# Kernel tuning notes

Hardware: AMD Instinct MI355X
Metric: run time of the kernel (lower is better)

The kernel has to match this reference:

```python
import jax, jax.numpy as jnp
import numpy as np

EPS = 1e-5

def _bn(x, g, b, axes):
    m = jnp.mean(x, axes, keepdims=True)
    v = jnp.var(x, axes, keepdims=True)
    return (x - m) * jax.lax.rsqrt(v + EPS) * g + b

def _fps(p, m):
    # farthest point sampling: p [B,N,3] -> int32 indices [B,m]
    B, N, _ = p.shape
    def step(carry, _):
        mind, last = carry
        lastp = jnp.take_along_axis(p, last[:, None, None], axis=1)[:, 0]  # [B,3]
        d = jnp.sum((p - lastp[:, None, :]) ** 2, axis=-1)                 # [B,N]
        mind = jnp.minimum(mind, d)
        nxt = jnp.argmax(mind, axis=1).astype(jnp.int32)
        return (mind, nxt), last
    init = (jnp.full((B, N), jnp.inf, p.dtype), jnp.zeros((B,), jnp.int32))
    _, idxs = jax.lax.scan(step, init, None, length=m)  # [m,B]
    return idxs.T

def _gather(x, idx):
    # x [B,N,C], idx [B,...] -> [B,...,C]
    B, C = x.shape[0], x.shape[-1]
    flat = idx.reshape(B, -1)
    out = jnp.take_along_axis(x, flat[:, :, None], axis=1)
    return out.reshape(idx.shape + (C,))

def _transition_down(p, h, W, g, b, stride, nsample):
    # p [B,N,3], h [B,N,C] -> new_p [B,N//stride,3], y [B,N//stride,Cout]
    B, N, _ = p.shape
    M = N // stride
    idx = _fps(p, M)
    new_p = _gather(p, idx)                                               # [B,M,3]
    d = jnp.sum((new_p[:, :, None, :] - p[:, None, :, :]) ** 2, axis=-1)  # [B,M,N]
    _, nidx = jax.lax.top_k(-d, nsample)                                  # [B,M,k]
    gp = _gather(p, nidx) - new_p[:, :, None, :]                          # rel xyz [B,M,k,3]
    gx = _gather(h, nidx)                                                 # [B,M,k,C]
    feat = jnp.concatenate([gp, gx], axis=-1)                             # with_xyz=True
    y = jnp.einsum('bmkc,cd->bmkd', feat, W)
    y = jax.nn.relu(_bn(y, g, b, (0, 1, 2)))
    return new_p, jnp.max(y, axis=2)                                      # MaxPool1d(nsample)

def _forward(x, W1, g1, b1, W2, g2, b2, W3, g3, b3, W4, g4, b4, W5, g5, b5,
             Wc1, bc1, gc1, hc1, Wc2, bc2, gc2, hc2, Wc3, bc3):
    p = x[..., :3]                                    # in_channels == 3 -> features = xyz
    h = jnp.einsum('bnc,cd->bnd', p, W1)
    h = jax.nn.relu(_bn(h, g1, b1, (0, 1)))           # enc1: stride=1
    p, h = _transition_down(p, h, W2, g2, b2, 4, 16)  # enc2
    p, h = _transition_down(p, h, W3, g3, b3, 4, 16)  # enc3
    p, h = _transition_down(p, h, W4, g4, b4, 4, 16)  # enc4
    p, h = _transition_down(p, h, W5, g5, b5, 4, 16)  # enc5
    z = jnp.mean(h, axis=1)                           # segment-mean pool -> [B,512]
    z = jax.nn.relu(_bn(z @ Wc1 + bc1, gc1, hc1, (0,)))   # Dropout = identity (eval)
    z = jax.nn.relu(_bn(z @ Wc2 + bc2, gc2, hc2, (0,)))
    return z @ Wc3 + bc3                              # [B,40]

def setup_inputs() -> dict:
    key = jax.random.key(0)
    ks = jax.random.split(key, 16)
    B, N = 16, 4096
    def lin(k, fi, fo):
        return (jax.random.normal(k, (fi, fo), jnp.float32) / np.sqrt(fi)).astype(jnp.float32)
    inp = {"x": jax.random.normal(ks[0], (B, N, 3), jnp.float32)}
    planes = [32, 64, 128, 256, 512]
    ins = [3, 3 + 32, 3 + 64, 3 + 128, 3 + 256]
    for i, (fi, fo) in enumerate(zip(ins, planes), start=1):
        inp[f"W{i}"] = lin(ks[i], fi, fo)
        inp[f"g{i}"] = jnp.ones((fo,), jnp.float32)
        inp[f"b{i}"] = jnp.zeros((fo,), jnp.float32)
    dims = [(512, 256), (256, 128), (128, 40)]
    for j, (fi, fo) in enumerate(dims, start=1):
        inp[f"Wc{j}"] = lin(ks[5 + j], fi, fo)
        inp[f"bc{j}"] = jnp.zeros((fo,), jnp.float32)
        if j < 3:
            inp[f"gc{j}"] = jnp.ones((fo,), jnp.float32)
            inp[f"hc{j}"] = jnp.zeros((fo,), jnp.float32)
    return inp

def reference(x, W1, g1, b1, W2, g2, b2, W3, g3, b3, W4, g4, b4, W5, g5, b5,
              Wc1, bc1, gc1, hc1, Wc2, bc2, gc2, hc2, Wc3, bc3):
    return _forward(x, W1, g1, b1, W2, g2, b2, W3, g3, b3, W4, g4, b4, W5, g5, b5,
                    Wc1, bc1, gc1, hc1, Wc2, bc2, gc2, hc2, Wc3, bc3)
```

## Files before the change

kernel.cpp:

```cpp
#include <hip/hip_runtime.h>
#include <math.h>
#include <float.h>

#define BN_EPS 1e-5f

__device__ __forceinline__ float sqdist_exact(float dx, float dy, float dz) {
  return __fadd_rn(__fadd_rn(__fmul_rn(dx, dx), __fmul_rn(dy, dy)), __fmul_rn(dz, dz));
}

__global__ void __launch_bounds__(256) mlp1_kernel(const float* __restrict__ x,
                                                   const float* __restrict__ W1,
                                                   float* __restrict__ h1, int rows) {
  int tid = blockIdx.x * 256 + threadIdx.x;
  int row = tid >> 5;
  int d = tid & 31;
  if (row >= rows) return;
  float x0 = x[row * 3 + 0], x1 = x[row * 3 + 1], x2 = x[row * 3 + 2];
  float acc = x0 * W1[d] + x1 * W1[32 + d] + x2 * W1[64 + d];
  h1[row * 32 + d] = acc;
}

__global__ void stats_kernel(const float* __restrict__ v, int n, int D,
                             float* __restrict__ partial) {
  int tid = blockIdx.x * blockDim.x + threadIdx.x;
  int stride = blockDim.x * gridDim.x;
  float s = 0.f, q = 0.f;
  for (int i = tid; i < n; i += stride) { float a = v[i]; s += a; q += a * a; }
  int c = tid % D;
  extern __shared__ float sm[];
  for (int i = threadIdx.x; i < 2 * D; i += blockDim.x) sm[i] = 0.f;
  __syncthreads();
  atomicAdd(&sm[c], s);
  atomicAdd(&sm[D + c], q);
  __syncthreads();
  for (int i = threadIdx.x; i < 2 * D; i += blockDim.x)
    atomicAdd(&partial[(blockIdx.x & 63) * 2 * D + i], sm[i]);
}

__global__ void finalize_kernel(const float* __restrict__ partial,
                                const float* __restrict__ g, const float* __restrict__ b,
                                float cnt, int D, float* __restrict__ ss) {
  int d = threadIdx.x;
  if (d >= D) return;
  float s = 0.f, q = 0.f;
  for (int j = 0; j < 64; j++) { s += partial[j * 2 * D + d]; q += partial[j * 2 * D + D + d]; }
  float mean = s / cnt;
  float var = q / cnt - mean * mean;
  var = fmaxf(var, 0.f);
  float sc = g[d] * rsqrtf(var + BN_EPS);
  ss[d] = sc;
  ss[D + d] = b[d] - mean * sc;
}

__global__ void bn_apply_kernel(float* __restrict__ vmax, const float* __restrict__ vmin,
                                const float* __restrict__ ss, int D, int n) {
  int tid = blockIdx.x * blockDim.x + threadIdx.x;
  int stride = blockDim.x * gridDim.x;
  for (int i = tid; i < n; i += stride) {
    int d = i % D;
    float sc = ss[d], sh = ss[D + d];
    float v = (sc >= 0.f) ? vmax[i] : vmin[i];
    vmax[i] = fmaxf(v * sc + sh, 0.f);
  }
}

#define DPP_STEP(CTRL)                                                                   \
  {                                                                                      \
    unsigned int nhi = (unsigned int)__builtin_amdgcn_update_dpp((int)khi, (int)khi,     \
                                                                 CTRL, 0xf, 0xf, false); \
    unsigned int nlo = (unsigned int)__builtin_amdgcn_update_dpp((int)klo, (int)klo,     \
                                                                 CTRL, 0xf, 0xf, false); \
    unsigned long long nk = (((unsigned long long)nhi) << 32) | nlo;                     \
    if (nk > wk) { wk = nk; khi = nhi; klo = nlo; }                                      \
  }

template <int P, int NW>
__global__ void __launch_bounds__(NW * 64) fps4_kernel(const float* __restrict__ p,
                                                       float* __restrict__ newp) {
  constexpr int BS = NW * 64;
  constexpr int N = P * BS;
  constexpr int M = N / 4;
  __shared__ float spts[N * 3];
  __shared__ float snew[NW > 1 ? M * 3 : 1];
  __shared__ unsigned long long slots[NW > 1 ? 2 * NW : 2];
  const int b = blockIdx.x;
  const int t = threadIdx.x;
  const int wv = t >> 6;
  const int lane = t & 63;
  const float* pb = p + (size_t)b * N * 3;
  float px[P], py[P], pz[P], md[P];
#pragma unroll
  for (int j = 0; j < P; j++) {
    int i = j * BS + t;
    float x = pb[3 * i], y = pb[3 * i + 1], z = pb[3 * i + 2];
    px[j] = x; py[j] = y; pz[j] = z; md[j] = INFINITY;
    spts[3 * i] = x; spts[3 * i + 1] = y; spts[3 * i + 2] = z;
  }
  float lx = pb[0], ly = pb[1], lz = pb[2];
  if (t == 0) {
    if constexpr (NW > 1) {
      snew[0] = lx; snew[1] = ly; snew[2] = lz;
    } else {
      newp[(size_t)b * M * 3 + 0] = lx;
      newp[(size_t)b * M * 3 + 1] = ly;
      newp[(size_t)b * M * 3 + 2] = lz;
    }
  }

  for (int r = 1; r < M; r++) {
    float bv; int bi;
    {
      float d0 = sqdist_exact(px[0] - lx, py[0] - ly, pz[0] - lz);
      float m0 = fminf(md[0], d0);
      md[0] = m0;
      bv = m0; bi = t;
    }
#pragma unroll
    for (int j = 1; j < P; j++) {
      float d = sqdist_exact(px[j] - lx, py[j] - ly, pz[j] - lz);
      float m = fminf(md[j], d);
      md[j] = m;
      if (m > bv) { bv = m; bi = j * BS + t; }
    }
    unsigned int khi = __float_as_uint(bv);
    unsigned int klo = ~(unsigned int)bi;
    unsigned long long wk = (((unsigned long long)khi) << 32) | klo;
    DPP_STEP(0x111);
    DPP_STEP(0x112);
    DPP_STEP(0x114);
    DPP_STEP(0x118);
    DPP_STEP(0x142);
    DPP_STEP(0x143);
    unsigned int gidx;
    if constexpr (NW == 1) {
      unsigned int wlo = (unsigned int)__builtin_amdgcn_readlane((int)wk, 63);
      gidx = ~wlo;
    } else {
      unsigned long long* base = slots + (r & 1) * NW;
      if (lane == 63) base[wv] = wk;
      __syncthreads();
      unsigned long long fk = base[0];
#pragma unroll
      for (int w = 1; w < NW; w++) {
        unsigned long long k2 = base[w];
        if (k2 > fk) fk = k2;
      }
      gidx = ~(unsigned int)fk;
    }
    lx = spts[3 * gidx];
    ly = spts[3 * gidx + 1];
    lz = spts[3 * gidx + 2];
    if (t == 0) {
      if constexpr (NW > 1) {
        snew[3 * r] = lx; snew[3 * r + 1] = ly; snew[3 * r + 2] = lz;
      } else {
        size_t o = ((size_t)b * M + r) * 3;
        newp[o] = lx; newp[o + 1] = ly; newp[o + 2] = lz;
      }
    }
  }
  if constexpr (NW > 1) {
    __syncthreads();
    for (int i = t; i < M * 3; i += BS) newp[(size_t)b * M * 3 + i] = snew[i];
  }
}

__global__ void __launch_bounds__(256) knn_kernel(const float* __restrict__ p,
                                                  const float* __restrict__ newp,
                                                  int N, int M, int BM,
                                                  int* __restrict__ nidx) {
  int gwid = (blockIdx.x * 256 + threadIdx.x) >> 6;
  int lane = threadIdx.x & 63;
  if (gwid >= BM) return;
  int b = gwid / M;
  const float* pb = p + (size_t)b * N * 3;
  float qx = newp[(size_t)gwid * 3], qy = newp[(size_t)gwid * 3 + 1], qz = newp[(size_t)gwid * 3 + 2];
  float bd[16];
  int bi[16];
#pragma unroll
  for (int s = 0; s < 16; s++) { bd[s] = INFINITY; bi[s] = 0x7FFFFFFF; }
  for (int c = lane; c < N; c += 64) {
    float d = sqdist_exact(pb[3 * c] - qx, pb[3 * c + 1] - qy, pb[3 * c + 2] - qz);
    if (d < bd[15]) {
      bd[15] = d; bi[15] = c;
#pragma unroll
      for (int s = 15; s >= 1; --s) {
        bool sw = bd[s] < bd[s - 1];
        if (sw) {
          float tf = bd[s]; bd[s] = bd[s - 1]; bd[s - 1] = tf;
          int ti = bi[s]; bi[s] = bi[s - 1]; bi[s - 1] = ti;
        }
      }
    }
  }
  int out = 0;
  for (int r = 0; r < 16; r++) {
    float v = bd[0]; int ii = bi[0];
    float mv = v; int mi = ii;
#pragma unroll
    for (int m = 1; m < 64; m <<= 1) {
      float v2 = __shfl_xor(mv, m);
      int i2 = __shfl_xor(mi, m);
      if (v2 < mv || (v2 == mv && i2 < mi)) { mv = v2; mi = i2; }
    }
    if (mi == ii) {
#pragma unroll
      for (int s = 0; s < 15; s++) { bd[s] = bd[s + 1]; bi[s] = bi[s + 1]; }
      bd[15] = INFINITY; bi[15] = 0x7FFFFFFF;
    }
    if (lane == r) out = mi;
  }
  if (lane < 16) nidx[(size_t)gwid * 16 + lane] = out;
}

__global__ void __launch_bounds__(256) gemm_kernel(
    const float* __restrict__ p, const float* __restrict__ h, const float* __restrict__ newp,
    const int* __restrict__ nidx, const float* __restrict__ W,
    float* __restrict__ ymax, float* __restrict__ ymin, float* __restrict__ partial,
    int N, int M, int BM, int Ch, int Cpad, int D, int Gseq) {
  extern __shared__ float sm[];
  int Ctot = Ch + 3;
  int TD = D < 256 ? D : 256;
  int Gpar = 256 / TD;
  float* sfeat = sm;
  float* sstat = sm + Gpar * 16 * Cpad;
  int t = threadIdx.x;
  for (int i = t; i < 2 * D; i += 256) sstat[i] = 0.f;
  int mloc = t / TD;
  int dbase = t % TD;
  int DV = D / TD;
  __syncthreads();
  for (int s = 0; s < Gseq; s++) {
    int grp0 = (blockIdx.x * Gseq + s) * Gpar;
    if (grp0 >= BM) break;
    int nf = Gpar * 16 * Cpad;
    for (int i = t; i < nf; i += 256) {
      int c = i % Cpad;
      int rk = i / Cpad;
      int k = rk & 15;
      int g = rk >> 4;
      int grp = grp0 + g;
      float val = 0.f;
      if (grp < BM && c < Ctot) {
        int b = grp / M;
        int nb = nidx[(size_t)grp * 16 + k];
        if (c < 3)
          val = p[((size_t)b * N + nb) * 3 + c] - newp[(size_t)grp * 3 + c];
        else
          val = h[((size_t)b * N + nb) * Ch + (c - 3)];
      }
      sfeat[i] = val;
    }
    __syncthreads();
    int grp = grp0 + mloc;
    bool act = grp < BM;
    const float* fr = sfeat + mloc * 16 * Cpad;
    for (int dv = 0; dv < DV; ++dv) {
      int d = dbase + (dv << 8);
      float acc[16];
#pragma unroll
      for (int k = 0; k < 16; k++) acc[k] = 0.f;
      for (int c = 0; c < Cpad; c += 4) {
        float w0 = (c < Ctot) ? W[(size_t)c * D + d] : 0.f;
        float w1 = (c + 1 < Ctot) ? W[(size_t)(c + 1) * D + d] : 0.f;
        float w2 = (c + 2 < Ctot) ? W[(size_t)(c + 2) * D + d] : 0.f;
        float w3 = (c + 3 < Ctot) ? W[(size_t)(c + 3) * D + d] : 0.f;
#pragma unroll
        for (int k = 0; k < 16; k++) {
          const float4 f = *reinterpret_cast<const float4*>(fr + k * Cpad + c);
          acc[k] += f.x * w0 + f.y * w1 + f.z * w2 + f.w * w3;
        }
      }
      if (act) {
        float ssum = 0.f, ssq = 0.f, amax = -INFINITY, amin = INFINITY;
#pragma unroll
        for (int k = 0; k < 16; k++) {
          float a = acc[k];
          ssum += a; ssq += a * a;
          amax = fmaxf(amax, a); amin = fminf(amin, a);
        }
        ymax[(size_t)grp * D + d] = amax;
        ymin[(size_t)grp * D + d] = amin;
        atomicAdd(&sstat[d], ssum);
        atomicAdd(&sstat[D + d], ssq);
      }
    }
    __syncthreads();
  }
  for (int i = t; i < 2 * D; i += 256)
    atomicAdd(&partial[(blockIdx.x & 63) * 2 * D + i], sstat[i]);
}

__global__ void __launch_bounds__(512) classifier_kernel(
    const float* __restrict__ h4,
    const float* __restrict__ Wc1, const float* __restrict__ bc1,
    const float* __restrict__ gc1, const float* __restrict__ hc1,
    const float* __restrict__ Wc2, const float* __restrict__ bc2,
    const float* __restrict__ gc2, const float* __restrict__ hc2,
    const float* __restrict__ Wc3, const float* __restrict__ bc3,
    float* __restrict__ out) {
  __shared__ float z[16 * 512];
  __shared__ float z1[16 * 256];
  __shared__ float z2[16 * 128];
  __shared__ float sc[256], sh[256];
  int t = threadIdx.x;
  for (int i = t; i < 16 * 512; i += 512) {
    int b = i >> 9, c = i & 511;
    float s = 0.f;
    for (int k = 0; k < 16; k++) s += h4[((size_t)b * 16 + k) * 512 + c];
    z[i] = s * (1.f / 16.f);
  }
  __syncthreads();
  for (int i = t; i < 16 * 256; i += 512) {
    int b = i >> 8, d = i & 255;
    float a = bc1[d];
    for (int c = 0; c < 512; c++) a += z[(b << 9) + c] * Wc1[c * 256 + d];
    z1[i] = a;
  }
  __syncthreads();
  if (t < 256) {
    float s = 0.f, q = 0.f;
    for (int b = 0; b < 16; b++) { float a = z1[(b << 8) + t]; s += a; q += a * a; }
    float mean = s * (1.f / 16.f);
    float var = fmaxf(q * (1.f / 16.f) - mean * mean, 0.f);
    float scl = gc1[t] * rsqrtf(var + BN_EPS);
    sc[t] = scl; sh[t] = hc1[t] - mean * scl;
  }
  __syncthreads();
  for (int i = t; i < 16 * 256; i += 512) {
    int d = i & 255;
    z1[i] = fmaxf(z1[i] * sc[d] + sh[d], 0.f);
  }
  __syncthreads();
  for (int i = t; i < 16 * 128; i += 512) {
    int b = i >> 7, d = i & 127;
    float a = bc2[d];
    for (int c = 0; c < 256; c++) a += z1[(b << 8) + c] * Wc2[c * 128 + d];
    z2[i] = a;
  }
  __syncthreads();
  if (t < 128) {
    float s = 0.f, q = 0.f;
    for (int b = 0; b < 16; b++) { float a = z2[(b << 7) + t]; s += a; q += a * a; }
    float mean = s * (1.f / 16.f);
    float var = fmaxf(q * (1.f / 16.f) - mean * mean, 0.f);
    float scl = gc2[t] * rsqrtf(var + BN_EPS);
    sc[t] = scl; sh[t] = hc2[t] - mean * scl;
  }
  __syncthreads();
  for (int i = t; i < 16 * 128; i += 512) {
    int d = i & 127;
    z2[i] = fmaxf(z2[i] * sc[d] + sh[d], 0.f);
  }
  __syncthreads();
  for (int i = t; i < 640; i += 512) {
    int b = i / 40, d = i % 40;
    float a = bc3[d];
    for (int c = 0; c < 128; c++) a += z2[(b << 7) + c] * Wc3[c * 40 + d];
    out[i] = a;
  }
}

extern "C" void kernel_launch(void* const* d_in, const int* in_sizes, int n_in,
                              void* d_out, int out_size, void* d_ws, size_t ws_size,
                              hipStream_t stream) {
  (void)in_sizes; (void)n_in; (void)out_size; (void)ws_size;
  const float* x   = (const float*)d_in[0];
  const float* W1  = (const float*)d_in[1];
  const float* g1  = (const float*)d_in[2];
  const float* b1  = (const float*)d_in[3];
  const float* W2  = (const float*)d_in[4];
  const float* g2  = (const float*)d_in[5];
  const float* b2  = (const float*)d_in[6];
  const float* W3  = (const float*)d_in[7];
  const float* g3  = (const float*)d_in[8];
  const float* b3  = (const float*)d_in[9];
  const float* W4  = (const float*)d_in[10];
  const float* g4  = (const float*)d_in[11];
  const float* b4  = (const float*)d_in[12];
  const float* W5  = (const float*)d_in[13];
  const float* g5  = (const float*)d_in[14];
  const float* b5  = (const float*)d_in[15];
  const float* Wc1 = (const float*)d_in[16];
  const float* bc1 = (const float*)d_in[17];
  const float* gc1 = (const float*)d_in[18];
  const float* hc1 = (const float*)d_in[19];
  const float* Wc2 = (const float*)d_in[20];
  const float* bc2 = (const float*)d_in[21];
  const float* gc2 = (const float*)d_in[22];
  const float* hc2 = (const float*)d_in[23];
  const float* Wc3 = (const float*)d_in[24];
  const float* bc3 = (const float*)d_in[25];
  float* out = (float*)d_out;

  float* ws = (float*)d_ws;
  float* HA   = ws;
  float* HB   = HA + 2097152;
  float* YMIN = HB + 1048576;
  float* NP1  = YMIN + 1048576;
  float* NP2  = NP1 + 49152;
  float* NP3  = NP2 + 12288;
  float* NP4  = NP3 + 3072;
  int*   NIDX = (int*)(NP4 + 768);
  float* PART = (float*)(NIDX + 262144);
  float* SS   = PART + 5 * 65536;

  hipMemsetAsync(PART, 0, 5 * 65536 * sizeof(float), stream);

  mlp1_kernel<<<(65536 * 32) / 256, 256, 0, stream>>>(x, W1, HA, 65536);
  stats_kernel<<<256, 256, 2 * 32 * sizeof(float), stream>>>(HA, 65536 * 32, 32, PART);
  finalize_kernel<<<1, 32, 0, stream>>>(PART, g1, b1, 65536.f, 32, SS);
  bn_apply_kernel<<<512, 256, 0, stream>>>(HA, HA, SS, 32, 65536 * 32);

  fps4_kernel<8, 8><<<16, 512, 0, stream>>>(x, NP1);
  knn_kernel<<<(16384 + 3) / 4, 256, 0, stream>>>(x, NP1, 4096, 1024, 16384, NIDX);
  gemm_kernel<<<512, 256, (4 * 16 * 36 + 2 * 64) * sizeof(float), stream>>>(
      x, HA, NP1, NIDX, W2, HB, YMIN, PART + 65536, 4096, 1024, 16384, 32, 36, 64, 8);
  finalize_kernel<<<1, 64, 0, stream>>>(PART + 65536, g2, b2, (float)(16384 * 16), 64, SS + 1024);
  bn_apply_kernel<<<512, 256, 0, stream>>>(HB, YMIN, SS + 1024, 64, 16384 * 64);

  fps4_kernel<16, 1><<<16, 64, 0, stream>>>(NP1, NP2);
  knn_kernel<<<(4096 + 3) / 4, 256, 0, stream>>>(NP1, NP2, 1024, 256, 4096, NIDX);
  gemm_kernel<<<512, 256, (2 * 16 * 68 + 2 * 128) * sizeof(float), stream>>>(
      NP1, HB, NP2, NIDX, W3, HA, YMIN, PART + 2 * 65536, 1024, 256, 4096, 64, 68, 128, 4);
  finalize_kernel<<<1, 128, 0, stream>>>(PART + 2 * 65536, g3, b3, (float)(4096 * 16), 128, SS + 2048);
  bn_apply_kernel<<<512, 256, 0, stream>>>(HA, YMIN, SS + 2048, 128, 4096 * 128);

  fps4_kernel<4, 1><<<16, 64, 0, stream>>>(NP2, NP3);
  knn_kernel<<<(1024 + 3) / 4, 256, 0, stream>>>(NP2, NP3, 256, 64, 1024, NIDX);
  gemm_kernel<<<512, 256, (16 * 132 + 2 * 256) * sizeof(float), stream>>>(
      NP2, HA, NP3, NIDX, W4, HB, YMIN, PART + 3 * 65536, 256, 64, 1024, 128, 132, 256, 2);
  finalize_kernel<<<1, 256, 0, stream>>>(PART + 3 * 65536, g4, b4, (float)(1024 * 16), 256, SS + 3072);
  bn_apply_kernel<<<512, 256, 0, stream>>>(HB, YMIN, SS + 3072, 256, 1024 * 256);

  fps4_kernel<1, 1><<<16, 64, 0, stream>>>(NP3, NP4);
  knn_kernel<<<(256 + 3) / 4, 256, 0, stream>>>(NP3, NP4, 64, 16, 256, NIDX);
  gemm_kernel<<<256, 256, (16 * 260 + 2 * 512) * sizeof(float), stream>>>(
      NP3, HB, NP4, NIDX, W5, HA, YMIN, PART + 4 * 65536, 64, 16, 256, 256, 260, 512, 1);
  finalize_kernel<<<1, 512, 0, stream>>>(PART + 4 * 65536, g5, b5, (float)(256 * 16), 512, SS + 4096);
  bn_apply_kernel<<<512, 256, 0, stream>>>(HA, YMIN, SS + 4096, 512, 256 * 512);

  classifier_kernel<<<1, 512, 0, stream>>>(HA, Wc1, bc1, gc1, hc1, Wc2, bc2, gc2, hc2, Wc3, bc3, out);
}
```

Before: 1.614 ms.

## Carry winner coordinates through FPS argmax reduction instead of shared-memory lookup

The farthest-point-sampling kernel now tracks the coordinates of each thread's best candidate and forwards them with the argmax key. Single-wave blocks read the winner's coordinates with readlane, and multi-wave blocks merge per-wave winners with DPP instead of a serial shared-memory scan. This removes the shared point copy and a dependent LDS load from every iteration. The first-level FPS also moves from 8 waves with 8 points per thread to 4 waves with 16 points per thread, adding register pressure and per-thread serial work in exchange for cheaper cross-wave reduction.

```diff
diff --git a/kernel.cpp b/kernel.cpp
--- a/kernel.cpp
+++ b/kernel.cpp
@@ -74,15 +74,34 @@
     if (nk > wk) { wk = nk; khi = nhi; klo = nlo; }                                      \
   }
 
+#define QP_MERGE(CTRL)                                                                    \
+  {                                                                                       \
+    unsigned int nhi = (unsigned int)__builtin_amdgcn_update_dpp((int)mhi, (int)mhi,      \
+                                                                 CTRL, 0xf, 0xf, false);  \
+    unsigned int nlo = (unsigned int)__builtin_amdgcn_update_dpp((int)mlo, (int)mlo,      \
+                                                                 CTRL, 0xf, 0xf, false);  \
+    int nxi = __builtin_amdgcn_update_dpp(__float_as_int(mx), __float_as_int(mx),         \
+                                          CTRL, 0xf, 0xf, false);                         \
+    int nyi = __builtin_amdgcn_update_dpp(__float_as_int(my2), __float_as_int(my2),       \
+                                          CTRL, 0xf, 0xf, false);                         \
+    int nzi = __builtin_amdgcn_update_dpp(__float_as_int(mz), __float_as_int(mz),         \
+                                          CTRL, 0xf, 0xf, false);                         \
+    unsigned long long ck = (((unsigned long long)mhi) << 32) | mlo;                      \
+    unsigned long long nk = (((unsigned long long)nhi) << 32) | nlo;                      \
+    if (nk > ck) {                                                                        \
+      mhi = nhi; mlo = nlo;                                                               \
+      mx = __int_as_float(nxi); my2 = __int_as_float(nyi); mz = __int_as_float(nzi);      \
+    }                                                                                     \
+  }
+
 template <int P, int NW>
-__global__ void __launch_bounds__(NW * 64) fps4_kernel(const float* __restrict__ p,
+__global__ void __launch_bounds__(NW * 64) fps5_kernel(const float* __restrict__ p,
                                                        float* __restrict__ newp) {
   constexpr int BS = NW * 64;
   constexpr int N = P * BS;
   constexpr int M = N / 4;
-  __shared__ float spts[N * 3];
-  __shared__ float snew[NW > 1 ? M * 3 : 1];
-  __shared__ unsigned long long slots[NW > 1 ? 2 * NW : 2];
+  __shared__ __align__(32) float slots[NW > 1 ? 2 * NW * 8 : 8];
+  __shared__ float snew[NW > 1 ? M * 3 : 3];
   const int b = blockIdx.x;
   const int t = threadIdx.x;
   const int wv = t >> 6;
@@ -92,9 +111,8 @@
 #pragma unroll
   for (int j = 0; j < P; j++) {
     int i = j * BS + t;
-    float x = pb[3 * i], y = pb[3 * i + 1], z = pb[3 * i + 2];
-    px[j] = x; py[j] = y; pz[j] = z; md[j] = INFINITY;
-    spts[3 * i] = x; spts[3 * i + 1] = y; spts[3 * i + 2] = z;
+    px[j] = pb[3 * i]; py[j] = pb[3 * i + 1]; pz[j] = pb[3 * i + 2];
+    md[j] = INFINITY;
   }
   float lx = pb[0], ly = pb[1], lz = pb[2];
   if (t == 0) {
@@ -108,22 +126,25 @@
   }
 
   for (int r = 1; r < M; r++) {
-    float bv; int bi;
+    float bv, bx, by, bz; int bi;
     {
       float d0 = sqdist_exact(px[0] - lx, py[0] - ly, pz[0] - lz);
       float m0 = fminf(md[0], d0);
       md[0] = m0;
-      bv = m0; bi = t;
+      bv = m0; bi = t; bx = px[0]; by = py[0]; bz = pz[0];
     }
 #pragma unroll
     for (int j = 1; j < P; j++) {
       float d = sqdist_exact(px[j] - lx, py[j] - ly, pz[j] - lz);
       float m = fminf(md[j], d);
       md[j] = m;
-      if (m > bv) { bv = m; bi = j * BS + t; }
+      if (m > bv) {
+        bv = m; bi = j * BS + t; bx = px[j]; by = py[j]; bz = pz[j];
+      }
     }
     unsigned int khi = __float_as_uint(bv);
     unsigned int klo = ~(unsigned int)bi;
+    const unsigned int myhi = khi, mylo = klo;
     unsigned long long wk = (((unsigned long long)khi) << 32) | klo;
     DPP_STEP(0x111);
     DPP_STEP(0x112);
@@ -131,31 +152,36 @@
     DPP_STEP(0x118);
     DPP_STEP(0x142);
     DPP_STEP(0x143);
-    unsigned int gidx;
+    unsigned int whi = (unsigned int)__builtin_amdgcn_readlane((int)(wk >> 32), 63);
+    unsigned int wlo = (unsigned int)__builtin_amdgcn_readlane((int)wk, 63);
+
     if constexpr (NW == 1) {
-      unsigned int wlo = (unsigned int)__builtin_amdgcn_readlane((int)wk, 63);
-      gidx = ~wlo;
-    } else {
-      unsigned long long* base = slots + (r & 1) * NW;
-      if (lane == 63) base[wv] = wk;
-      __syncthreads();
-      unsigned long long fk = base[0];
-#pragma unroll
-      for (int w = 1; w < NW; w++) {
-        unsigned long long k2 = base[w];
-        if (k2 > fk) fk = k2;
-      }
-      gidx = ~(unsigned int)fk;
-    }
-    lx = spts[3 * gidx];
-    ly = spts[3 * gidx + 1];
-    lz = spts[3 * gidx + 2];
-    if (t == 0) {
-      if constexpr (NW > 1) {
-        snew[3 * r] = lx; snew[3 * r + 1] = ly; snew[3 * r + 2] = lz;
-      } else {
+      int owner = (int)((~wlo) & 63u);
+      lx = __int_as_float(__builtin_amdgcn_readlane(__float_as_int(bx), owner));
+      ly = __int_as_float(__builtin_amdgcn_readlane(__float_as_int(by), owner));
+      lz = __int_as_float(__builtin_amdgcn_readlane(__float_as_int(bz), owner));
+      if (t == 0) {
         size_t o = ((size_t)b * M + r) * 3;
         newp[o] = lx; newp[o + 1] = ly; newp[o + 2] = lz;
+      }
+    } else {
+      float* base = slots + (r & 1) * NW * 8;
+      if (myhi == whi && mylo == wlo) {
+        float4 v = make_float4(__uint_as_float(whi), __uint_as_float(wlo), bx, by);
+        *reinterpret_cast<float4*>(base + wv * 8) = v;
+        base[wv * 8 + 4] = bz;
+      }
+      __syncthreads();
+      const float* sl = base + (lane & (NW - 1)) * 8;
+      const float4 s4 = *reinterpret_cast<const float4*>(sl);
+      float mz = sl[4];
+      unsigned int mhi = __float_as_uint(s4.x), mlo = __float_as_uint(s4.y);
+      float mx = s4.z, my2 = s4.w;
+      if constexpr (NW >= 2) QP_MERGE(0xB1);
+      if constexpr (NW >= 4) QP_MERGE(0x4E);
+      lx = mx; ly = my2; lz = mz;
+      if (t == 0) {
+        snew[3 * r] = lx; snew[3 * r + 1] = ly; snew[3 * r + 2] = lz;
       }
     }
   }
@@ -412,28 +438,28 @@
   finalize_kernel<<<1, 32, 0, stream>>>(PART, g1, b1, 65536.f, 32, SS);
   bn_apply_kernel<<<512, 256, 0, stream>>>(HA, HA, SS, 32, 65536 * 32);
 
-  fps4_kernel<8, 8><<<16, 512, 0, stream>>>(x, NP1);
+  fps5_kernel<16, 4><<<16, 256, 0, stream>>>(x, NP1);
   knn_kernel<<<(16384 + 3) / 4, 256, 0, stream>>>(x, NP1, 4096, 1024, 16384, NIDX);
   gemm_kernel<<<512, 256, (4 * 16 * 36 + 2 * 64) * sizeof(float), stream>>>(
       x, HA, NP1, NIDX, W2, HB, YMIN, PART + 65536, 4096, 1024, 16384, 32, 36, 64, 8);
   finalize_kernel<<<1, 64, 0, stream>>>(PART + 65536, g2, b2, (float)(16384 * 16), 64, SS + 1024);
   bn_apply_kernel<<<512, 256, 0, stream>>>(HB, YMIN, SS + 1024, 64, 16384 * 64);
 
-  fps4_kernel<16, 1><<<16, 64, 0, stream>>>(NP1, NP2);
+  fps5_kernel<16, 1><<<16, 64, 0, stream>>>(NP1, NP2);
   knn_kernel<<<(4096 + 3) / 4, 256, 0, stream>>>(NP1, NP2, 1024, 256, 4096, NIDX);
   gemm_kernel<<<512, 256, (2 * 16 * 68 + 2 * 128) * sizeof(float), stream>>>(
       NP1, HB, NP2, NIDX, W3, HA, YMIN, PART + 2 * 65536, 1024, 256, 4096, 64, 68, 128, 4);
   finalize_kernel<<<1, 128, 0, stream>>>(PART + 2 * 65536, g3, b3, (float)(4096 * 16), 128, SS + 2048);
   bn_apply_kernel<<<512, 256, 0, stream>>>(HA, YMIN, SS + 2048, 128, 4096 * 128);
 
-  fps4_kernel<4, 1><<<16, 64, 0, stream>>>(NP2, NP3);
+  fps5_kernel<4, 1><<<16, 64, 0, stream>>>(NP2, NP3);
   knn_kernel<<<(1024 + 3) / 4, 256, 0, stream>>>(NP2, NP3, 256, 64, 1024, NIDX);
   gemm_kernel<<<512, 256, (16 * 132 + 2 * 256) * sizeof(float), stream>>>(
       NP2, HA, NP3, NIDX, W4, HB, YMIN, PART + 3 * 65536, 256, 64, 1024, 128, 132, 256, 2);
   finalize_kernel<<<1, 256, 0, stream>>>(PART + 3 * 65536, g4, b4, (float)(1024 * 16), 256, SS + 3072);
   bn_apply_kernel<<<512, 256, 0, stream>>>(HB, YMIN, SS + 3072, 256, 1024 * 256);
 
-  fps4_kernel<1, 1><<<16, 64, 0, stream>>>(NP3, NP4);
+  fps5_kernel<1, 1><<<16, 64, 0, stream>>>(NP3, NP4);
   knn_kernel<<<(256 + 3) / 4, 256, 0, stream>>>(NP3, NP4, 64, 16, 256, NIDX);
   gemm_kernel<<<256, 256, (16 * 260 + 2 * 512) * sizeof(float), stream>>>(
       NP3, HB, NP4, NIDX, W5, HA, YMIN, PART + 4 * 65536, 64, 16, 256, 256, 260, 512, 1);
```

Result: slower. 1.904 ms (+18.0%).

## Fuse whole encoder into persistent megakernel overlapping FPS with worker stages

Applied to the files above, without the earlier changes.

Replaces the roughly twenty separate launches with one persistent kernel. Sixteen blocks run all four farthest-point-sampling levels back to back, chaining levels 2-4 in a single wavefront via readlane. The remaining 240 worker blocks run the MLP, kNN, gather-GEMM and batch-norm stages, separated by device-wide atomic barriers and per-level FPS ready flags. This lets the serial FPS chain overlap the MLP/BN and kNN/GEMM work and removes launch gaps. The cost is a deadlock risk if all 256 blocks are not co-resident, spin-wait overhead, and a fixed worker count for every stage.

```diff
diff --git a/kernel.cpp b/kernel.cpp
--- a/kernel.cpp
+++ b/kernel.cpp
@@ -3,65 +3,12 @@
 #include <float.h>
 
 #define BN_EPS 1e-5f
+#define WB 240
+#define FB 16
+#define TPB 512
 
 __device__ __forceinline__ float sqdist_exact(float dx, float dy, float dz) {
   return __fadd_rn(__fadd_rn(__fmul_rn(dx, dx), __fmul_rn(dy, dy)), __fmul_rn(dz, dz));
-}
-
-__global__ void __launch_bounds__(256) mlp1_kernel(const float* __restrict__ x,
-                                                   const float* __restrict__ W1,
-                                                   float* __restrict__ h1, int rows) {
-  int tid = blockIdx.x * 256 + threadIdx.x;
-  int row = tid >> 5;
-  int d = tid & 31;
-  if (row >= rows) return;
-  float x0 = x[row * 3 + 0], x1 = x[row * 3 + 1], x2 = x[row * 3 + 2];
-  float acc = x0 * W1[d] + x1 * W1[32 + d] + x2 * W1[64 + d];
-  h1[row * 32 + d] = acc;
-}
-
-__global__ void stats_kernel(const float* __restrict__ v, int n, int D,
-                             float* __restrict__ partial) {
-  int tid = blockIdx.x * blockDim.x + threadIdx.x;
-  int stride = blockDim.x * gridDim.x;
-  float s = 0.f, q = 0.f;
-  for (int i = tid; i < n; i += stride) { float a = v[i]; s += a; q += a * a; }
-  int c = tid % D;
-  extern __shared__ float sm[];
-  for (int i = threadIdx.x; i < 2 * D; i += blockDim.x) sm[i] = 0.f;
-  __syncthreads();
-  atomicAdd(&sm[c], s);
-  atomicAdd(&sm[D + c], q);
-  __syncthreads();
-  for (int i = threadIdx.x; i < 2 * D; i += blockDim.x)
-    atomicAdd(&partial[(blockIdx.x & 63) * 2 * D + i], sm[i]);
-}
-
-__global__ void finalize_kernel(const float* __restrict__ partial,
-                                const float* __restrict__ g, const float* __restrict__ b,
-                                float cnt, int D, float* __restrict__ ss) {
-  int d = threadIdx.x;
-  if (d >= D) return;
-  float s = 0.f, q = 0.f;
-  for (int j = 0; j < 64; j++) { s += partial[j * 2 * D + d]; q += partial[j * 2 * D + D + d]; }
-  float mean = s / cnt;
-  float var = q / cnt - mean * mean;
-  var = fmaxf(var, 0.f);
-  float sc = g[d] * rsqrtf(var + BN_EPS);
-  ss[d] = sc;
-  ss[D + d] = b[d] - mean * sc;
-}
-
-__global__ void bn_apply_kernel(float* __restrict__ vmax, const float* __restrict__ vmin,
-                                const float* __restrict__ ss, int D, int n) {
-  int tid = blockIdx.x * blockDim.x + threadIdx.x;
-  int stride = blockDim.x * gridDim.x;
-  for (int i = tid; i < n; i += stride) {
-    int d = i % D;
-    float sc = ss[d], sh = ss[D + d];
-    float v = (sc >= 0.f) ? vmax[i] : vmin[i];
-    vmax[i] = fmaxf(v * sc + sh, 0.f);
-  }
 }
 
 #define DPP_STEP(CTRL)                                                                   \
@@ -74,40 +21,108 @@
     if (nk > wk) { wk = nk; khi = nhi; klo = nlo; }                                      \
   }
 
-template <int P, int NW>
-__global__ void __launch_bounds__(NW * 64) fps4_kernel(const float* __restrict__ p,
-                                                       float* __restrict__ newp) {
-  constexpr int BS = NW * 64;
-  constexpr int N = P * BS;
-  constexpr int M = N / 4;
-  __shared__ float spts[N * 3];
-  __shared__ float snew[NW > 1 ? M * 3 : 1];
-  __shared__ unsigned long long slots[NW > 1 ? 2 * NW : 2];
-  const int b = blockIdx.x;
-  const int t = threadIdx.x;
-  const int wv = t >> 6;
-  const int lane = t & 63;
-  const float* pb = p + (size_t)b * N * 3;
-  float px[P], py[P], pz[P], md[P];
-#pragma unroll
-  for (int j = 0; j < P; j++) {
+struct MegaParams {
+  const float* x;
+  const float *W1, *g1, *b1;
+  const float *W2, *g2, *b2;
+  const float *W3, *g3, *b3;
+  const float *W4, *g4, *b4;
+  const float *W5, *g5, *b5;
+  float *HA, *HB, *YMIN;
+  float *NP1, *NP2, *NP3, *NP4;
+  int *NIDX1, *NIDX2, *NIDX3, *NIDX4;
+  float* PART;
+  int* SYNC;
+};
+
+__device__ __forceinline__ void worker_bar(int* cnt, int phase, int t) {
+  __syncthreads();
+  if (t == 0) {
+    __threadfence();
+    __hip_atomic_fetch_add(&cnt[phase], 1, __ATOMIC_RELEASE, __HIP_MEMORY_SCOPE_AGENT);
+    while (__hip_atomic_load(&cnt[phase], __ATOMIC_ACQUIRE, __HIP_MEMORY_SCOPE_AGENT) < WB)
+      __builtin_amdgcn_s_sleep(16);
+  }
+  __syncthreads();
+}
+
+__device__ __forceinline__ void wait_np(int* np, int k, int t) {
+  if (t == 0)
+    while (__hip_atomic_load(&np[k], __ATOMIC_ACQUIRE, __HIP_MEMORY_SCOPE_AGENT) < FB)
+      __builtin_amdgcn_s_sleep(16);
+  __syncthreads();
+}
+
+template <int PP>
+__device__ void fps_w0(const float* src, float* dstG, float* dstL, int lane, int* flag) {
+  constexpr int N = PP * 64, M = N / 4;
+  float px[PP], py[PP], pz[PP], md[PP];
+#pragma unroll
+  for (int j = 0; j < PP; j++) {
+    int i = j * 64 + lane;
+    px[j] = src[3 * i]; py[j] = src[3 * i + 1]; pz[j] = src[3 * i + 2];
+    md[j] = INFINITY;
+  }
+  float lx = src[0], ly = src[1], lz = src[2];
+  if (lane == 0) {
+    dstG[0] = lx; dstG[1] = ly; dstG[2] = lz;
+    if (dstL) { dstL[0] = lx; dstL[1] = ly; dstL[2] = lz; }
+  }
+  for (int r = 1; r < M; r++) {
+    float bv, bx, by, bz; int bi;
+    {
+      float d0 = sqdist_exact(px[0] - lx, py[0] - ly, pz[0] - lz);
+      float m0 = fminf(md[0], d0);
+      md[0] = m0;
+      bv = m0; bi = lane; bx = px[0]; by = py[0]; bz = pz[0];
+    }
+#pragma unroll
+    for (int j = 1; j < PP; j++) {
+      float d = sqdist_exact(px[j] - lx, py[j] - ly, pz[j] - lz);
+      float m = fminf(md[j], d);
+      md[j] = m;
+      if (m > bv) { bv = m; bi = j * 64 + lane; bx = px[j]; by = py[j]; bz = pz[j]; }
+    }
+    unsigned int khi = __float_as_uint(bv);
+    unsigned int klo = ~(unsigned int)bi;
+    unsigned long long wk = (((unsigned long long)khi) << 32) | klo;
+    DPP_STEP(0x111); DPP_STEP(0x112); DPP_STEP(0x114);
+    DPP_STEP(0x118); DPP_STEP(0x142); DPP_STEP(0x143);
+    unsigned int wlo = (unsigned int)__builtin_amdgcn_readlane((int)wk, 63);
+    int owner = (int)((~wlo) & 63u);
+    lx = __int_as_float(__builtin_amdgcn_readlane(__float_as_int(bx), owner));
+    ly = __int_as_float(__builtin_amdgcn_readlane(__float_as_int(by), owner));
+    lz = __int_as_float(__builtin_amdgcn_readlane(__float_as_int(bz), owner));
+    if (lane == 0) {
+      dstG[3 * r] = lx; dstG[3 * r + 1] = ly; dstG[3 * r + 2] = lz;
+      if (dstL) { dstL[3 * r] = lx; dstL[3 * r + 1] = ly; dstL[3 * r + 2] = lz; }
+    }
+  }
+  if (lane == 0) {
+    __threadfence();
+    __hip_atomic_fetch_add(flag, 1, __ATOMIC_RELEASE, __HIP_MEMORY_SCOPE_AGENT);
+  }
+}
+
+__device__ void fps_role(const MegaParams& P, float* smem, int b, int t) {
+  constexpr int P1 = 8, BS = 512, N1 = 4096, M1 = 1024;
+  float* spts = smem;
+  float* snew = smem + 12288;
+  unsigned long long* slots = (unsigned long long*)(smem + 15360);
+  const int wv = t >> 6, lane = t & 63;
+  const float* pb = P.x + (size_t)b * N1 * 3;
+  float px[P1], py[P1], pz[P1], md[P1];
+#pragma unroll
+  for (int j = 0; j < P1; j++) {
     int i = j * BS + t;
-    float x = pb[3 * i], y = pb[3 * i + 1], z = pb[3 * i + 2];
-    px[j] = x; py[j] = y; pz[j] = z; md[j] = INFINITY;
-    spts[3 * i] = x; spts[3 * i + 1] = y; spts[3 * i + 2] = z;
+    float xx = pb[3 * i], yy = pb[3 * i + 1], zz = pb[3 * i + 2];
+    px[j] = xx; py[j] = yy; pz[j] = zz; md[j] = INFINITY;
+    spts[3 * i] = xx; spts[3 * i + 1] = yy; spts[3 * i + 2] = zz;
   }
   float lx = pb[0], ly = pb[1], lz = pb[2];
-  if (t == 0) {
-    if constexpr (NW > 1) {
-      snew[0] = lx; snew[1] = ly; snew[2] = lz;
-    } else {
-      newp[(size_t)b * M * 3 + 0] = lx;
-      newp[(size_t)b * M * 3 + 1] = ly;
-      newp[(size_t)b * M * 3 + 2] = lz;
-    }
-  }
-
-  for (int r = 1; r < M; r++) {
+  if (t == 0) { snew[0] = lx; snew[1] = ly; snew[2] = lz; }
+
+  for (int r = 1; r < M1; r++) {
     float bv; int bi;
     {
       float d0 = sqdist_exact(px[0] - lx, py[0] - ly, pz[0] - lz);
@@ -116,7 +131,7 @@
       bv = m0; bi = t;
     }
 #pragma unroll
-    for (int j = 1; j < P; j++) {
+    for (int j = 1; j < P1; j++) {
       float d = sqdist_exact(px[j] - lx, py[j] - ly, pz[j] - lz);
       float m = fminf(md[j], d);
       md[j] = m;
@@ -125,116 +140,140 @@
     unsigned int khi = __float_as_uint(bv);
     unsigned int klo = ~(unsigned int)bi;
     unsigned long long wk = (((unsigned long long)khi) << 32) | klo;
-    DPP_STEP(0x111);
-    DPP_STEP(0x112);
-    DPP_STEP(0x114);
-    DPP_STEP(0x118);
-    DPP_STEP(0x142);
-    DPP_STEP(0x143);
-    unsigned int gidx;
-    if constexpr (NW == 1) {
-      unsigned int wlo = (unsigned int)__builtin_amdgcn_readlane((int)wk, 63);
-      gidx = ~wlo;
-    } else {
-      unsigned long long* base = slots + (r & 1) * NW;
-      if (lane == 63) base[wv] = wk;
-      __syncthreads();
-      unsigned long long fk = base[0];
-#pragma unroll
-      for (int w = 1; w < NW; w++) {
-        unsigned long long k2 = base[w];
-        if (k2 > fk) fk = k2;
-      }
-      gidx = ~(unsigned int)fk;
-    }
-    lx = spts[3 * gidx];
-    ly = spts[3 * gidx + 1];
-    lz = spts[3 * gidx + 2];
-    if (t == 0) {
-      if constexpr (NW > 1) {
-        snew[3 * r] = lx; snew[3 * r + 1] = ly; snew[3 * r + 2] = lz;
-      } else {
-        size_t o = ((size_t)b * M + r) * 3;
-        newp[o] = lx; newp[o + 1] = ly; newp[o + 2] = lz;
-      }
-    }
-  }
-  if constexpr (NW > 1) {
+    DPP_STEP(0x111); DPP_STEP(0x112); DPP_STEP(0x114);
+    DPP_STEP(0x118); DPP_STEP(0x142); DPP_STEP(0x143);
+    unsigned long long* base = slots + (r & 1) * 8;
+    if (lane == 63) base[wv] = wk;
     __syncthreads();
-    for (int i = t; i < M * 3; i += BS) newp[(size_t)b * M * 3 + i] = snew[i];
-  }
-}
-
-__global__ void __launch_bounds__(256) knn_kernel(const float* __restrict__ p,
-                                                  const float* __restrict__ newp,
-                                                  int N, int M, int BM,
-                                                  int* __restrict__ nidx) {
-  int gwid = (blockIdx.x * 256 + threadIdx.x) >> 6;
-  int lane = threadIdx.x & 63;
-  if (gwid >= BM) return;
-  int b = gwid / M;
-  const float* pb = p + (size_t)b * N * 3;
-  float qx = newp[(size_t)gwid * 3], qy = newp[(size_t)gwid * 3 + 1], qz = newp[(size_t)gwid * 3 + 2];
-  float bd[16];
-  int bi[16];
-#pragma unroll
-  for (int s = 0; s < 16; s++) { bd[s] = INFINITY; bi[s] = 0x7FFFFFFF; }
-  for (int c = lane; c < N; c += 64) {
-    float d = sqdist_exact(pb[3 * c] - qx, pb[3 * c + 1] - qy, pb[3 * c + 2] - qz);
-    if (d < bd[15]) {
-      bd[15] = d; bi[15] = c;
-#pragma unroll
-      for (int s = 15; s >= 1; --s) {
-        bool sw = bd[s] < bd[s - 1];
-        if (sw) {
-          float tf = bd[s]; bd[s] = bd[s - 1]; bd[s - 1] = tf;
-          int ti = bi[s]; bi[s] = bi[s - 1]; bi[s - 1] = ti;
+    unsigned long long fk = base[0];
+#pragma unroll
+    for (int w = 1; w < 8; w++) {
+      unsigned long long k2 = base[w];
+      if (k2 > fk) fk = k2;
+    }
+    unsigned int gidx = ~(unsigned int)fk;
+    lx = spts[3 * gidx]; ly = spts[3 * gidx + 1]; lz = spts[3 * gidx + 2];
+    if (t == 0) { snew[3 * r] = lx; snew[3 * r + 1] = ly; snew[3 * r + 2] = lz; }
+  }
+  __syncthreads();
+  for (int i = t; i < M1 * 3; i += BS) P.NP1[(size_t)b * M1 * 3 + i] = snew[i];
+  __syncthreads();
+  if (t == 0) {
+    __threadfence();
+    __hip_atomic_fetch_add(&P.SYNC[0], 1, __ATOMIC_RELEASE, __HIP_MEMORY_SCOPE_AGENT);
+  }
+  if (t < 64) {
+    float* snewB = smem;
+    float* snewC = smem + 1024;
+    fps_w0<16>(snew, P.NP2 + (size_t)b * 256 * 3, snewB, lane, &P.SYNC[1]);
+    fps_w0<4>(snewB, P.NP3 + (size_t)b * 64 * 3, snewC, lane, &P.SYNC[2]);
+    fps_w0<1>(snewC, P.NP4 + (size_t)b * 16 * 3, (float*)0, lane, &P.SYNC[3]);
+  }
+}
+
+__device__ void mlp_w(const MegaParams& P, float* smem, int wid, int t, int bslot) {
+  float s = 0.f, q = 0.f;
+  int tid0 = wid * TPB + t;
+  int d0 = tid0 & 31;
+  for (int i = tid0; i < 65536 * 32; i += WB * TPB) {
+    int row = i >> 5, d = i & 31;
+    float x0 = P.x[row * 3], x1 = P.x[row * 3 + 1], x2 = P.x[row * 3 + 2];
+    float a = x0 * P.W1[d] + x1 * P.W1[32 + d] + x2 * P.W1[64 + d];
+    P.HA[i] = a; s += a; q += a * a;
+  }
+  float* sm2 = smem;
+  for (int i = t; i < 64; i += TPB) sm2[i] = 0.f;
+  __syncthreads();
+  atomicAdd(&sm2[d0], s);
+  atomicAdd(&sm2[32 + d0], q);
+  __syncthreads();
+  for (int i = t; i < 64; i += TPB) atomicAdd(&P.PART[bslot * 64 + i], sm2[i]);
+}
+
+__device__ void ss_compute(const float* partial, const float* g, const float* bb,
+                           float cnt, int D, float* ssl, int t) {
+  for (int d = t; d < D; d += TPB) {
+    float s = 0.f, q = 0.f;
+    for (int j = 0; j < 64; j++) { s += partial[j * 2 * D + d]; q += partial[j * 2 * D + D + d]; }
+    float mean = s / cnt;
+    float var = fmaxf(q / cnt - mean * mean, 0.f);
+    float sc = g[d] * rsqrtf(var + BN_EPS);
+    ssl[d] = sc; ssl[D + d] = bb[d] - mean * sc;
+  }
+  __syncthreads();
+}
+
+__device__ void bn_w(float* vmax, const float* vmin, const float* ssl, int D, int n,
+                     int wid, int t) {
+  for (int i = wid * TPB + t; i < n; i += WB * TPB) {
+    int d = i & (D - 1);
+    float sc = ssl[d], sh = ssl[D + d];
+    float v = (sc >= 0.f) ? vmax[i] : vmin[i];
+    vmax[i] = fmaxf(v * sc + sh, 0.f);
+  }
+}
+
+__device__ void knn_w(const float* p, const float* newp, int N, int M, int BM,
+                      int* nidx, int wid, int t) {
+  int gw = wid * 8 + (t >> 6);
+  int lane = t & 63;
+  for (int q = gw; q < BM; q += WB * 8) {
+    int b = q / M;
+    const float* pb = p + (size_t)b * N * 3;
+    float qx = newp[(size_t)q * 3], qy = newp[(size_t)q * 3 + 1], qz = newp[(size_t)q * 3 + 2];
+    float bd[16]; int bi[16];
+#pragma unroll
+    for (int s = 0; s < 16; s++) { bd[s] = INFINITY; bi[s] = 0x7FFFFFFF; }
+    for (int c = lane; c < N; c += 64) {
+      float d = sqdist_exact(pb[3 * c] - qx, pb[3 * c + 1] - qy, pb[3 * c + 2] - qz);
+      if (d < bd[15]) {
+        bd[15] = d; bi[15] = c;
+#pragma unroll
+        for (int s = 15; s >= 1; --s) {
+          if (bd[s] < bd[s - 1]) {
+            float tf = bd[s]; bd[s] = bd[s - 1]; bd[s - 1] = tf;
+            int ti = bi[s]; bi[s] = bi[s - 1]; bi[s - 1] = ti;
+          }
         }
       }
     }
-  }
-  int out = 0;
-  for (int r = 0; r < 16; r++) {
-    float v = bd[0]; int ii = bi[0];
-    float mv = v; int mi = ii;
-#pragma unroll
-    for (int m = 1; m < 64; m <<= 1) {
-      float v2 = __shfl_xor(mv, m);
-      int i2 = __shfl_xor(mi, m);
-      if (v2 < mv || (v2 == mv && i2 < mi)) { mv = v2; mi = i2; }
-    }
-    if (mi == ii) {
-#pragma unroll
-      for (int s = 0; s < 15; s++) { bd[s] = bd[s + 1]; bi[s] = bi[s + 1]; }
-      bd[15] = INFINITY; bi[15] = 0x7FFFFFFF;
-    }
-    if (lane == r) out = mi;
-  }
-  if (lane < 16) nidx[(size_t)gwid * 16 + lane] = out;
-}
-
-__global__ void __launch_bounds__(256) gemm_kernel(
-    const float* __restrict__ p, const float* __restrict__ h, const float* __restrict__ newp,
-    const int* __restrict__ nidx, const float* __restrict__ W,
-    float* __restrict__ ymax, float* __restrict__ ymin, float* __restrict__ partial,
-    int N, int M, int BM, int Ch, int Cpad, int D, int Gseq) {
-  extern __shared__ float sm[];
+    int out = 0;
+    for (int r = 0; r < 16; r++) {
+      float v = bd[0]; int ii = bi[0];
+      float mv = v; int mi = ii;
+#pragma unroll
+      for (int m = 1; m < 64; m <<= 1) {
+        float v2 = __shfl_xor(mv, m);
+        int i2 = __shfl_xor(mi, m);
+        if (v2 < mv || (v2 == mv && i2 < mi)) { mv = v2; mi = i2; }
+      }
+      if (mi == ii) {
+#pragma unroll
+        for (int s = 0; s < 15; s++) { bd[s] = bd[s + 1]; bi[s] = bi[s + 1]; }
+        bd[15] = INFINITY; bi[15] = 0x7FFFFFFF;
+      }
+      if (lane == r) out = mi;
+    }
+    if (lane < 16) nidx[(size_t)q * 16 + lane] = out;
+  }
+}
+
+__device__ void gemm_w(const float* p, const float* h, const float* newp,
+                       const int* nidx, const float* W,
+                       float* ymax, float* ymin, float* partial,
+                       int N, int M, int BM, int Ch, int Cpad, int D,
+                       int wid, int t, float* smem, int bslot) {
   int Ctot = Ch + 3;
-  int TD = D < 256 ? D : 256;
-  int Gpar = 256 / TD;
-  float* sfeat = sm;
-  float* sstat = sm + Gpar * 16 * Cpad;
-  int t = threadIdx.x;
-  for (int i = t; i < 2 * D; i += 256) sstat[i] = 0.f;
-  int mloc = t / TD;
-  int dbase = t % TD;
-  int DV = D / TD;
-  __syncthreads();
-  for (int s = 0; s < Gseq; s++) {
-    int grp0 = (blockIdx.x * Gseq + s) * Gpar;
-    if (grp0 >= BM) break;
+  int Gpar = TPB / D;
+  float* sfeat = smem;
+  float* sstat = smem + 8192;
+  for (int i = t; i < 2 * D; i += TPB) sstat[i] = 0.f;
+  int mloc = t / D;
+  int d = t % D;
+  __syncthreads();
+  for (int grp0 = wid * Gpar; grp0 < BM; grp0 += WB * Gpar) {
     int nf = Gpar * 16 * Cpad;
-    for (int i = t; i < nf; i += 256) {
+    for (int i = t; i < nf; i += TPB) {
       int c = i % Cpad;
       int rk = i / Cpad;
       int k = rk & 15;
@@ -255,40 +294,96 @@
     int grp = grp0 + mloc;
     bool act = grp < BM;
     const float* fr = sfeat + mloc * 16 * Cpad;
-    for (int dv = 0; dv < DV; ++dv) {
-      int d = dbase + (dv << 8);
-      float acc[16];
-#pragma unroll
-      for (int k = 0; k < 16; k++) acc[k] = 0.f;
-      for (int c = 0; c < Cpad; c += 4) {
-        float w0 = (c < Ctot) ? W[(size_t)c * D + d] : 0.f;
-        float w1 = (c + 1 < Ctot) ? W[(size_t)(c + 1) * D + d] : 0.f;
-        float w2 = (c + 2 < Ctot) ? W[(size_t)(c + 2) * D + d] : 0.f;
-        float w3 = (c + 3 < Ctot) ? W[(size_t)(c + 3) * D + d] : 0.f;
-#pragma unroll
-        for (int k = 0; k < 16; k++) {
-          const float4 f = *reinterpret_cast<const float4*>(fr + k * Cpad + c);
-          acc[k] += f.x * w0 + f.y * w1 + f.z * w2 + f.w * w3;
-        }
+    float acc[16];
+#pragma unroll
+    for (int k = 0; k < 16; k++) acc[k] = 0.f;
+    for (int c = 0; c < Cpad; c += 4) {
+      float w0 = (c < Ctot) ? W[(size_t)c * D + d] : 0.f;
+      float w1 = (c + 1 < Ctot) ? W[(size_t)(c + 1) * D + d] : 0.f;
+      float w2 = (c + 2 < Ctot) ? W[(size_t)(c + 2) * D + d] : 0.f;
+      float w3 = (c + 3 < Ctot) ? W[(size_t)(c + 3) * D + d] : 0.f;
+#pragma unroll
+      for (int k = 0; k < 16; k++) {
+        const float4 f = *reinterpret_cast<const float4*>(fr + k * Cpad + c);
+        acc[k] += f.x * w0 + f.y * w1 + f.z * w2 + f.w * w3;
       }
-      if (act) {
-        float ssum = 0.f, ssq = 0.f, amax = -INFINITY, amin = INFINITY;
-#pragma unroll
-        for (int k = 0; k < 16; k++) {
-          float a = acc[k];
-          ssum += a; ssq += a * a;
-          amax = fmaxf(amax, a); amin = fminf(amin, a);
-        }
-        ymax[(size_t)grp * D + d] = amax;
-        ymin[(size_t)grp * D + d] = amin;
-        atomicAdd(&sstat[d], ssum);
-        atomicAdd(&sstat[D + d], ssq);
+    }
+    if (act) {
+      float ssum = 0.f, ssq = 0.f, amax = -INFINITY, amin = INFINITY;
+#pragma unroll
+      for (int k = 0; k < 16; k++) {
+        float a = acc[k];
+        ssum += a; ssq += a * a;
+        amax = fmaxf(amax, a); amin = fminf(amin, a);
       }
+      ymax[(size_t)grp * D + d] = amax;
+      ymin[(size_t)grp * D + d] = amin;
+      atomicAdd(&sstat[d], ssum);
+      atomicAdd(&sstat[D + d], ssq);
     }
     __syncthreads();
   }
-  for (int i = t; i < 2 * D; i += 256)
-    atomicAdd(&partial[(blockIdx.x & 63) * 2 * D + i], sstat[i]);
+  for (int i = t; i < 2 * D; i += TPB)
+    atomicAdd(&partial[bslot * 2 * D + i], sstat[i]);
+}
+
+__device__ void worker_role(const MegaParams& P, float* smem, int wid, int t, int bslot) {
+  int* np = P.SYNC;
+  int* cnt = P.SYNC + 4;
+  float* ssl = smem;
+
+  mlp_w(P, smem, wid, t, bslot);
+  worker_bar(cnt, 0, t);
+  ss_compute(P.PART, P.g1, P.b1, 65536.f, 32, ssl, t);
+  bn_w(P.HA, P.HA, ssl, 32, 65536 * 32, wid, t);
+  worker_bar(cnt, 1, t);
+
+  wait_np(np, 0, t);
+  knn_w(P.x, P.NP1, 4096, 1024, 16384, P.NIDX1, wid, t);
+  worker_bar(cnt, 2, t);
+  gemm_w(P.x, P.HA, P.NP1, P.NIDX1, P.W2, P.HB, P.YMIN, P.PART + 65536,
+         4096, 1024, 16384, 32, 36, 64, wid, t, smem, bslot);
+  worker_bar(cnt, 3, t);
+
+  ss_compute(P.PART + 65536, P.g2, P.b2, (float)(16384 * 16), 64, ssl, t);
+  bn_w(P.HB, P.YMIN, ssl, 64, 16384 * 64, wid, t);
+  wait_np(np, 1, t);
+  knn_w(P.NP1, P.NP2, 1024, 256, 4096, P.NIDX2, wid, t);
+  worker_bar(cnt, 4, t);
+  gemm_w(P.NP1, P.HB, P.NP2, P.NIDX2, P.W3, P.HA, P.YMIN, P.PART + 2 * 65536,
+         1024, 256, 4096, 64, 68, 128, wid, t, smem, bslot);
+  worker_bar(cnt, 5, t);
+
+  ss_compute(P.PART + 2 * 65536, P.g3, P.b3, (float)(4096 * 16), 128, ssl, t);
+  bn_w(P.HA, P.YMIN, ssl, 128, 4096 * 128, wid, t);
+  wait_np(np, 2, t);
+  knn_w(P.NP2, P.NP3, 256, 64, 1024, P.NIDX3, wid, t);
+  worker_bar(cnt, 6, t);
+  gemm_w(P.NP2, P.HA, P.NP3, P.NIDX3, P.W4, P.HB, P.YMIN, P.PART + 3 * 65536,
+         256, 64, 1024, 128, 132, 256, wid, t, smem, bslot);
+  worker_bar(cnt, 7, t);
+
+  ss_compute(P.PART + 3 * 65536, P.g4, P.b4, (float)(1024 * 16), 256, ssl, t);
+  bn_w(P.HB, P.YMIN, ssl, 256, 1024 * 256, wid, t);
+  wait_np(np, 3, t);
+  knn_w(P.NP3, P.NP4, 64, 16, 256, P.NIDX4, wid, t);
+  worker_bar(cnt, 8, t);
+  gemm_w(P.NP3, P.HB, P.NP4, P.NIDX4, P.W5, P.HA, P.YMIN, P.PART + 4 * 65536,
+         64, 16, 256, 256, 260, 512, wid, t, smem, bslot);
+  worker_bar(cnt, 9, t);
+
+  ss_compute(P.PART + 4 * 65536, P.g5, P.b5, (float)(256 * 16), 512, ssl, t);
+  bn_w(P.HA, P.YMIN, ssl, 512, 256 * 512, wid, t);
+}
+
+__global__ void __launch_bounds__(TPB, 4) mega_kernel(MegaParams P) {
+  __shared__ __align__(16) float smem[15872];
+  int t = threadIdx.x;
+  if (blockIdx.x < FB) {
+    fps_role(P, smem, blockIdx.x, t);
+  } else {
+    worker_role(P, smem, blockIdx.x - FB, t, blockIdx.x & 63);
+  }
 }
 
 __global__ void __launch_bounds__(512) classifier_kernel(
@@ -365,22 +460,13 @@
                               void* d_out, int out_size, void* d_ws, size_t ws_size,
                               hipStream_t stream) {
   (void)in_sizes; (void)n_in; (void)out_size; (void)ws_size;
-  const float* x   = (const float*)d_in[0];
-  const float* W1  = (const float*)d_in[1];
-  const float* g1  = (const float*)d_in[2];
-  const float* b1  = (const float*)d_in[3];
-  const float* W2  = (const float*)d_in[4];
-  const float* g2  = (const float*)d_in[5];
-  const float* b2  = (const float*)d_in[6];
-  const float* W3  = (const float*)d_in[7];
-  const float* g3  = (const float*)d_in[8];
-  const float* b3  = (const float*)d_in[9];
-  const float* W4  = (const float*)d_in[10];
-  const float* g4  = (const float*)d_in[11];
-  const float* b4  = (const float*)d_in[12];
-  const float* W5  = (const float*)d_in[13];
-  const float* g5  = (const float*)d_in[14];
-  const float* b5  = (const float*)d_in[15];
+  MegaParams P;
+  P.x  = (const float*)d_in[0];
+  P.W1 = (const float*)d_in[1];  P.g1 = (const float*)d_in[2];  P.b1 = (const float*)d_in[3];
+  P.W2 = (const float*)d_in[4];  P.g2 = (const float*)d_in[5];  P.b2 = (const float*)d_in[6];
+  P.W3 = (const float*)d_in[7];  P.g3 = (const float*)d_in[8];  P.b3 = (const float*)d_in[9];
+  P.W4 = (const float*)d_in[10]; P.g4 = (const float*)d_in[11]; P.b4 = (const float*)d_in[12];
+  P.W5 = (const float*)d_in[13]; P.g5 = (const float*)d_in[14]; P.b5 = (const float*)d_in[15];
   const float* Wc1 = (const float*)d_in[16];
   const float* bc1 = (const float*)d_in[17];
   const float* gc1 = (const float*)d_in[18];
@@ -394,51 +480,24 @@
   float* out = (float*)d_out;
 
   float* ws = (float*)d_ws;
-  float* HA   = ws;
-  float* HB   = HA + 2097152;
-  float* YMIN = HB + 1048576;
-  float* NP1  = YMIN + 1048576;
-  float* NP2  = NP1 + 49152;
-  float* NP3  = NP2 + 12288;
-  float* NP4  = NP3 + 3072;
-  int*   NIDX = (int*)(NP4 + 768);
-  float* PART = (float*)(NIDX + 262144);
-  float* SS   = PART + 5 * 65536;
-
-  hipMemsetAsync(PART, 0, 5 * 65536 * sizeof(float), stream);
-
-  mlp1_kernel<<<(65536 * 32) / 256, 256, 0, stream>>>(x, W1, HA, 65536);
-  stats_kernel<<<256, 256, 2 * 32 * sizeof(float), stream>>>(HA, 65536 * 32, 32, PART);
-  finalize_kernel<<<1, 32, 0, stream>>>(PART, g1, b1, 65536.f, 32, SS);
-  bn_apply_kernel<<<512, 256, 0, stream>>>(HA, HA, SS, 32, 65536 * 32);
-
-  fps4_kernel<8, 8><<<16, 512, 0, stream>>>(x, NP1);
-  knn_kernel<<<(16384 + 3) / 4, 256, 0, stream>>>(x, NP1, 4096, 1024, 16384, NIDX);
-  gemm_kernel<<<512, 256, (4 * 16 * 36 + 2 * 64) * sizeof(float), stream>>>(
-      x, HA, NP1, NIDX, W2, HB, YMIN, PART + 65536, 4096, 1024, 16384, 32, 36, 64, 8);
-  finalize_kernel<<<1, 64, 0, stream>>>(PART + 65536, g2, b2, (float)(16384 * 16), 64, SS + 1024);
-  bn_apply_kernel<<<512, 256, 0, stream>>>(HB, YMIN, SS + 1024, 64, 16384 * 64);
-
-  fps4_kernel<16, 1><<<16, 64, 0, stream>>>(NP1, NP2);
-  knn_kernel<<<(4096 + 3) / 4, 256, 0, stream>>>(NP1, NP2, 1024, 256, 4096, NIDX);
-  gemm_kernel<<<512, 256, (2 * 16 * 68 + 2 * 128) * sizeof(float), stream>>>(
-      NP1, HB, NP2, NIDX, W3, HA, YMIN, PART + 2 * 65536, 1024, 256, 4096, 64, 68, 128, 4);
-  finalize_kernel<<<1, 128, 0, stream>>>(PART + 2 * 65536, g3, b3, (float)(4096 * 16), 128, SS + 2048);
-  bn_apply_kernel<<<512, 256, 0, stream>>>(HA, YMIN, SS + 2048, 128, 4096 * 128);
-
-  fps4_kernel<4, 1><<<16, 64, 0, stream>>>(NP2, NP3);
-  knn_kernel<<<(1024 + 3) / 4, 256, 0, stream>>>(NP2, NP3, 256, 64, 1024, NIDX);
-  gemm_kernel<<<512, 256, (16 * 132 + 2 * 256) * sizeof(float), stream>>>(
-      NP2, HA, NP3, NIDX, W4, HB, YMIN, PART + 3 * 65536, 256, 64, 1024, 128, 132, 256, 2);
-  finalize_kernel<<<1, 256, 0, stream>>>(PART + 3 * 65536, g4, b4, (float)(1024 * 16), 256, SS + 3072);
-  bn_apply_kernel<<<512, 256, 0, stream>>>(HB, YMIN, SS + 3072, 256, 1024 * 256);
-
-  fps4_kernel<1, 1><<<16, 64, 0, stream>>>(NP3, NP4);
-  knn_kernel<<<(256 + 3) / 4, 256, 0, stream>>>(NP3, NP4, 64, 16, 256, NIDX);
-  gemm_kernel<<<256, 256, (16 * 260 + 2 * 512) * sizeof(float), stream>>>(
-      NP3, HB, NP4, NIDX, W5, HA, YMIN, PART + 4 * 65536, 64, 16, 256, 256, 260, 512, 1);
-  finalize_kernel<<<1, 512, 0, stream>>>(PART + 4 * 65536, g5, b5, (float)(256 * 16), 512, SS + 4096);
-  bn_apply_kernel<<<512, 256, 0, stream>>>(HA, YMIN, SS + 4096, 512, 256 * 512);
-
-  classifier_kernel<<<1, 512, 0, stream>>>(HA, Wc1, bc1, gc1, hc1, Wc2, bc2, gc2, hc2, Wc3, bc3, out);
-}
+  P.HA   = ws;
+  P.HB   = P.HA + 2097152;
+  P.YMIN = P.HB + 1048576;
+  P.NP1  = P.YMIN + 1048576;
+  P.NP2  = P.NP1 + 49152;
+  P.NP3  = P.NP2 + 12288;
+  P.NP4  = P.NP3 + 3072;
+  P.NIDX1 = (int*)(P.NP4 + 768);
+  P.NIDX2 = P.NIDX1 + 262144;
+  P.NIDX3 = P.NIDX2 + 65536;
+  P.NIDX4 = P.NIDX3 + 16384;
+  P.PART  = (float*)(P.NIDX4 + 4096);
+  P.SYNC  = (int*)(P.PART + 5 * 65536);
+
+  hipMemsetAsync(P.PART, 0, (5 * 65536 + 32) * sizeof(float), stream);
+
+  mega_kernel<<<FB + WB, TPB, 0, stream>>>(P);
+
+  classifier_kernel<<<1, 512, 0, stream>>>(P.HA, Wc1, bc1, gc1, hc1,
+                                           Wc2, bc2, gc2, hc2, Wc3, bc3, out);
+}
```

After: 2.377 ms. 47.2% more time.
